# Kernel tuning notes

Hardware: AMD Instinct MI355X
Metric: run time of the kernel (lower is better)

Reference implementation:

```python
import jax, jax.numpy as jnp
import numpy as np

NSAMPLE = 64
RADIUS = 0.05
HMIN = -0.02
HMAX_LIST = (0.01, 0.02, 0.03, 0.04)
BN_EPS = 1e-5
MLP_DIMS = (3, 64, 128, 256)


def setup_inputs() -> dict:
    key = jax.random.key(0)
    ks = jax.random.split(key, 16)
    B, S, N = 2, 1024, 20000
    # points and seeds in a [0,0.5]^3 box so 0.05-radius cylinders are non-empty
    seed_xyz = jax.random.uniform(ks[0], (B, S, 3), dtype=jnp.float32) * 0.5
    pointcloud = jax.random.uniform(ks[1], (B, N, 3), dtype=jnp.float32) * 0.5
    m = jax.random.normal(ks[2], (B, S, 3, 3), dtype=jnp.float32)
    vp_rot, _ = jnp.linalg.qr(m)  # proper-ish random rotations per seed
    inp = {"seed_xyz": seed_xyz, "pointcloud": pointcloud, "vp_rot": vp_rot}
    for i in range(3):
        cin, cout = MLP_DIMS[i], MLP_DIMS[i + 1]
        inp[f"w{i+1}"] = jax.random.normal(ks[3 + i], (cout, cin), dtype=jnp.float32) * (1.0 / np.sqrt(cin))
        inp[f"gamma{i+1}"] = 1.0 + 0.1 * jax.random.normal(ks[6 + i], (cout,), dtype=jnp.float32)
        inp[f"beta{i+1}"] = 0.1 * jax.random.normal(ks[9 + i], (cout,), dtype=jnp.float32)
        inp[f"mean{i+1}"] = 0.1 * jax.random.normal(ks[12 + i], (cout,), dtype=jnp.float32)
        inp[f"var{i+1}"] = jax.random.uniform(ks[15], (cout,), minval=0.5, maxval=1.5, dtype=jnp.float32)
    return inp


def _cylinder_group(rel_rot, hmax):
    # rel_rot: (B, S, N, 3) point coords relative to each seed, in the seed (approach) frame.
    # Cylinder axis = x (approach vector): keep points with hmin < x < hmax and y^2+z^2 < r^2.
    N = rel_rot.shape[2]
    x, y, z = rel_rot[..., 0], rel_rot[..., 1], rel_rot[..., 2]
    mask = (y * y + z * z < RADIUS * RADIUS) & (x > HMIN) & (x < hmax)  # (B,S,N)
    # first NSAMPLE valid indices (ascending), padded with the first valid index (0 if none)
    score = jnp.where(mask, jnp.arange(N, dtype=jnp.int32), N)
    neg_vals, _ = jax.lax.top_k(-score, NSAMPLE)
    idx = -neg_vals  # (B,S,NSAMPLE), value N marks missing
    first = jnp.where(idx[..., :1] >= N, 0, idx[..., :1])
    idx = jnp.where(idx >= N, first, idx)
    return jnp.take_along_axis(rel_rot, idx[..., None], axis=2)  # (B,S,NSAMPLE,3)


def _bn_relu(h, gamma, beta, mean, var):
    inv = gamma / jnp.sqrt(var + BN_EPS)
    s = inv[None, :, None, None]
    b = (beta - mean * inv)[None, :, None, None]
    return jax.nn.relu(h * s + b)


def _forward(seed_xyz, pointcloud, vp_rot, layers):
    B, S, _ = seed_xyz.shape
    D = len(HMAX_LIST)
    rel = pointcloud[:, None, :, :] - seed_xyz[:, :, None, :]        # (B,S,N,3)
    rel_rot = jnp.einsum('bsnc,bscd->bsnd', rel, vp_rot)             # rotate into seed frame (rel @ rot)
    grouped = jnp.stack([_cylinder_group(rel_rot, h) for h in HMAX_LIST], axis=2)  # (B,S,D,ns,3)
    feat = jnp.transpose(grouped, (0, 4, 1, 2, 3)).reshape(B, 3, S * D, NSAMPLE)   # (B,3,S*D,ns)
    for (w, g, be, m, v) in layers:
        feat = _bn_relu(jnp.einsum('oc,bcpn->bopn', w, feat), g, be, m, v)
    vp = jnp.max(feat, axis=-1)                                       # max-pool over nsample
    return vp.reshape(B, -1, S, D)                                    # (B,256,S,D)


def reference(seed_xyz, pointcloud, vp_rot,
              w1, gamma1, beta1, mean1, var1,
              w2, gamma2, beta2, mean2, var2,
              w3, gamma3, beta3, mean3, var3):
    layers = [(w1, gamma1, beta1, mean1, var1),
              (w2, gamma2, beta2, mean2, var2),
              (w3, gamma3, beta3, mean3, var3)]
    return _forward(seed_xyz, pointcloud, vp_rot, layers)
```

## Files before the change

kernel.cpp:

```cpp
#include <hip/hip_runtime.h>

#define NPTS   20000
#define NCHUNK 313

typedef __bf16 bf16x8 __attribute__((ext_vector_type(8)));
typedef float  f32x4  __attribute__((ext_vector_type(4)));

__device__ __forceinline__ unsigned short f2b(float f) {
    __bf16 h = (__bf16)f;
    union { __bf16 h; unsigned short s; } u; u.h = h; return u.s;
}
__device__ __forceinline__ unsigned int pk2(float a, float b) {
    return (unsigned int)f2b(a) | ((unsigned int)f2b(b) << 16);
}

#define WS_BINNED    0
#define WS_PARTHIST  640000
#define WS_COUNTS    721920
#define WS_OFFSETS   726016
#define WS_FLAGS     730112
#define WS_W2P       730368
#define WS_W3P       746752
#define WS_W1E       812288
#define WS_B1E       813056
#define WS_B2E       813312
#define WS_B3E       813824


__global__ __launch_bounds__(512)
void hist_prepack_kernel(const float* __restrict__ pointcloud,
                const float* __restrict__ w1,
                const float* __restrict__ g1,  const float* __restrict__ be1,
                const float* __restrict__ mn1, const float* __restrict__ vr1,
                const float* __restrict__ w2,
                const float* __restrict__ g2,  const float* __restrict__ be2,
                const float* __restrict__ mn2, const float* __restrict__ vr2,
                const float* __restrict__ w3,
                const float* __restrict__ g3,  const float* __restrict__ be3,
                const float* __restrict__ mn3, const float* __restrict__ vr3,
                unsigned int* __restrict__ parthist,
                unsigned short* __restrict__ w2p,
                unsigned short* __restrict__ w3p,
                float* __restrict__ w1e_g, float* __restrict__ b1e_g,
                float* __restrict__ b2e_g, float* __restrict__ b3e_g)
{
    __shared__ unsigned int h[512];
    const int blk = blockIdx.x;
    const int b   = blk / 20;
    const int p   = blk % 20;
    const int tid = threadIdx.x;
    const int gid = blk * 512 + tid;

    for (int e = gid; e < 8192; e += 20480) {
        int row = e >> 6;
        float inv = g2[row] / sqrtf(vr2[row] + 1e-5f);
        w2p[e] = f2b(w2[e] * inv);
    }
    for (int e = gid; e < 32768; e += 20480) {
        int row = e >> 7;
        float inv = g3[row] / sqrtf(vr3[row] + 1e-5f);
        w3p[e] = f2b(w3[e] * inv);
    }
    if (gid < 64) {
        float inv = g1[gid] / sqrtf(vr1[gid] + 1e-5f);
        w1e_g[gid*3+0] = inv * w1[gid*3+0];
        w1e_g[gid*3+1] = inv * w1[gid*3+1];
        w1e_g[gid*3+2] = inv * w1[gid*3+2];
        b1e_g[gid]     = be1[gid] - mn1[gid] * inv;
    }
    if (gid < 128) {
        float inv = g2[gid] / sqrtf(vr2[gid] + 1e-5f);
        b2e_g[gid] = be2[gid] - mn2[gid] * inv;
    }
    if (gid < 256) {
        float inv = g3[gid] / sqrtf(vr3[gid] + 1e-5f);
        b3e_g[gid] = be3[gid] - mn3[gid] * inv;
    }

    h[tid] = 0;
    __syncthreads();

    const float* base = pointcloud + (b * NPTS + p * 1000) * 3;
    for (int i = tid; i < 1000; i += 512) {
        float x = base[i*3+0], y = base[i*3+1], z = base[i*3+2];
        int cx = min(7, (int)(x * 16.0f));
        int cy = min(7, (int)(y * 16.0f));
        int cz = min(7, (int)(z * 16.0f));
        atomicAdd(&h[(cz * 8 + cy) * 8 + cx], 1u);
    }
    __syncthreads();

    parthist[blk * 512 + tid] = h[tid];
}

__global__ __launch_bounds__(512)
void scan_kernel(const unsigned int* __restrict__ parthist,
                 unsigned int* __restrict__ counts,
                 unsigned int* __restrict__ offsets)
{
    __shared__ unsigned int scanv[512];
    const int b   = blockIdx.x;
    const int tid = threadIdx.x;

    unsigned int cnt = 0;
    #pragma unroll
    for (int pp = 0; pp < 20; ++pp)
        cnt += parthist[(b * 20 + pp) * 512 + tid];

    scanv[tid] = cnt;
    __syncthreads();
    #pragma unroll
    for (int off = 1; off < 512; off <<= 1) {
        unsigned int v = 0;
        if (tid >= off) v = scanv[tid - off];
        __syncthreads();
        scanv[tid] += v;
        __syncthreads();
    }
    unsigned int excl = scanv[tid] - cnt;
    counts [b * 512 + tid] = cnt;
    offsets[b * 512 + tid] = b * NPTS + excl;
}

__global__ __launch_bounds__(512)
void scatter_kernel(const float* __restrict__ pointcloud,
                    const unsigned int* __restrict__ parthist,
                    const unsigned int* __restrict__ offsets,
                    float4* __restrict__ binned)
{
    __shared__ unsigned int cur[512];
    const int blk = blockIdx.x;
    const int b   = blk / 20;
    const int p   = blk % 20;
    const int tid = threadIdx.x;

    unsigned int partial = 0;
    for (int pp = 0; pp < p; ++pp)
        partial += parthist[(b * 20 + pp) * 512 + tid];
    cur[tid] = offsets[b * 512 + tid] + partial;
    __syncthreads();

    const float* base = pointcloud + (b * NPTS + p * 1000) * 3;
    for (int i = tid; i < 1000; i += 512) {
        float x = base[i*3+0], y = base[i*3+1], z = base[i*3+2];
        int cx = min(7, (int)(x * 16.0f));
        int cy = min(7, (int)(y * 16.0f));
        int cz = min(7, (int)(z * 16.0f));
        int cid = (cz * 8 + cy) * 8 + cx;
        unsigned int slot = atomicAdd(&cur[cid], 1u);
        binned[slot] = make_float4(x, y, z, __int_as_float(p * 1000 + i));
    }
}

struct __align__(16) SMemF {
    union {
        struct {
            unsigned int bm[4][640];
            int cstart[64];
            int ccnt[64];
        } a;
        struct {
            unsigned short h1[64][72];
            unsigned short h2[64][136];
        } b;
    } u;
    int    idxs[4][64];
    float  w1e[64][3];
    float  b1e[64];
};

__global__ __launch_bounds__(256, 2)
void fused_kernel(const float* __restrict__ seed_xyz,
                  const float* __restrict__ pointcloud,
                  const float* __restrict__ vp_rot,
                  const unsigned int* __restrict__ counts,
                  const unsigned int* __restrict__ offsets,
                  const float4* __restrict__ binned,
                  const unsigned short* __restrict__ w2p,
                  const unsigned short* __restrict__ w3p,
                  const float* __restrict__ w1e_g, const float* __restrict__ b1e_g,
                  const float* __restrict__ b2e_g, const float* __restrict__ b3e_g,
                  float* __restrict__ out)
{
    __shared__ SMemF sm;
    const int tid = threadIdx.x;
    const int wv  = tid >> 6;
    const int ln  = tid & 63;
    const int q   = ln >> 4;
    const int l15 = ln & 15;

    const int blk = blockIdx.x;
    const int i8  = blk >> 3;
    const int s   = (blk & 7) * 128 + (i8 & 127);
    const int b   = i8 >> 7;
    const int bs  = b * 1024 + s;

    if (tid < 64) {
        sm.w1e[tid][0] = w1e_g[tid*3+0];
        sm.w1e[tid][1] = w1e_g[tid*3+1];
        sm.w1e[tid][2] = w1e_g[tid*3+2];
        sm.b1e[tid]    = b1e_g[tid];
    }

    {
        unsigned int* bmp = &sm.u.a.bm[0][0];
        #pragma unroll
        for (int i = 0; i < 10; ++i) bmp[tid + i * 256] = 0;
    }

    const float sx = seed_xyz[bs*3+0];
    const float sy = seed_xyz[bs*3+1];
    const float sz = seed_xyz[bs*3+2];
    const float R00 = vp_rot[bs*9+0], R01 = vp_rot[bs*9+1], R02 = vp_rot[bs*9+2];
    const float R10 = vp_rot[bs*9+3], R11 = vp_rot[bs*9+4], R12 = vp_rot[bs*9+5];
    const float R20 = vp_rot[bs*9+6], R21 = vp_rot[bs*9+7], R22 = vp_rot[bs*9+8];

    const int lx = max(0, (int)floorf((sx - 0.066f) * 16.f));
    const int hx = min(7, (int)floorf((sx + 0.066f) * 16.f));
    const int ly = max(0, (int)floorf((sy - 0.066f) * 16.f));
    const int hy = min(7, (int)floorf((sy + 0.066f) * 16.f));
    const int lz = max(0, (int)floorf((sz - 0.066f) * 16.f));
    const int hz = min(7, (int)floorf((sz + 0.066f) * 16.f));
    const int nx = hx - lx + 1, ny = hy - ly + 1, nz = hz - lz + 1;
    const int ncell = nx * ny * nz;

    if (tid < ncell) {
        int cz = lz + tid / (nx * ny);
        int rem = tid % (nx * ny);
        int cy = ly + rem / nx;
        int cx = lx + rem % nx;
        int cid = (cz * 8 + cy) * 8 + cx;
        sm.u.a.cstart[tid] = (int)offsets[b * 512 + cid];
        sm.u.a.ccnt[tid]   = (int)counts [b * 512 + cid];
    }
    __syncthreads();

    {
        #pragma clang fp contract(off)
        for (int k = wv; k < ncell; k += 4) {
            const int base = sm.u.a.cstart[k];
            const int cnt  = sm.u.a.ccnt[k];
            for (int i = ln; i < cnt; i += 64) {
                float4 pt = binned[base + i];
                float rx = pt.x - sx, ry = pt.y - sy, rz = pt.z - sz;
                float x = (rx*R00 + ry*R10) + rz*R20;
                float y = (rx*R01 + ry*R11) + rz*R21;
                float z = (rx*R02 + ry*R12) + rz*R22;
                if (((y*y + z*z) < 0.0025f) && (x > -0.02f) && (x < 0.04f)) {
                    int n = __float_as_int(pt.w);
                    unsigned int bit = 1u << (n & 31);
                    int wi = n >> 5;
                    if (x < 0.01f) atomicOr(&sm.u.a.bm[0][wi], bit);
                    if (x < 0.02f) atomicOr(&sm.u.a.bm[1][wi], bit);
                    if (x < 0.03f) atomicOr(&sm.u.a.bm[2][wi], bit);
                    atomicOr(&sm.u.a.bm[3][wi], bit);
                }
            }
        }
    }
    __syncthreads();

    {
        const int d = wv;
        int carry = 0;
        for (int r = 0; r < 5 && carry < 64; ++r) {
            int c = r*64 + ln;
            unsigned long long w = 0ULL;
            if (c < NCHUNK)
                w = ((unsigned long long)sm.u.a.bm[d][2*c+1] << 32)
                  |  (unsigned long long)sm.u.a.bm[d][2*c];
            int wc = __popcll(w);
            int incl = wc;
            #pragma unroll
            for (int off = 1; off < 64; off <<= 1) {
                int t = __shfl_up(incl, off);
                if (ln >= off) incl += t;
            }
            int rank  = carry + incl - wc;
            int total = __shfl(incl, 63);
            while (w && rank < 64) {
                int bp = __builtin_ctzll(w);
                w &= w - 1;
                sm.idxs[d][rank] = c*64 + bp;
                ++rank;
            }
            carry += total;
        }
        int cnt = carry < 64 ? carry : 64;
        int first = (cnt > 0) ? sm.idxs[d][0] : 0;
        if (ln >= cnt) sm.idxs[d][ln] = first;
    }

    bf16x8 aw2[2][2];
    #pragma unroll
    for (int m = 0; m < 2; ++m) {
        int row = (wv*2+m)*16 + l15;
        #pragma unroll
        for (int kk = 0; kk < 2; ++kk)
            aw2[m][kk] = *(const bf16x8*)(w2p + row*64 + kk*32 + q*8);
    }

    __syncthreads();

    auto do_l1 = [&](int d) {
        int n = sm.idxs[d][ln];
        const float* p = pointcloud + (b*NPTS + n)*3;
        float x0, x1, x2;
        {
            #pragma clang fp contract(off)
            float rx = p[0] - sx, ry = p[1] - sy, rz = p[2] - sz;
            x0 = (rx*R00 + ry*R10) + rz*R20;
            x1 = (rx*R01 + ry*R11) + rz*R21;
            x2 = (rx*R02 + ry*R12) + rz*R22;
        }
        unsigned int pk[8];
        #pragma unroll
        for (int i = 0; i < 8; ++i) {
            int ch = wv*16 + i*2;
            float ha = fmaf(x0, sm.w1e[ch][0],
                       fmaf(x1, sm.w1e[ch][1],
                       fmaf(x2, sm.w1e[ch][2], sm.b1e[ch])));
            float hb = fmaf(x0, sm.w1e[ch+1][0],
                       fmaf(x1, sm.w1e[ch+1][1],
                       fmaf(x2, sm.w1e[ch+1][2], sm.b1e[ch+1])));
            pk[i] = pk2(fmaxf(ha, 0.f), fmaxf(hb, 0.f));
        }
        *(uint4*)&sm.u.b.h1[ln][wv*16 + 0] = make_uint4(pk[0], pk[1], pk[2], pk[3]);
        *(uint4*)&sm.u.b.h1[ln][wv*16 + 8] = make_uint4(pk[4], pk[5], pk[6], pk[7]);
    };

    do_l1(0);
    __syncthreads();

    for (int d = 0; d < 4; ++d) {
        {
            f32x4 binit2[2];
            #pragma unroll
            for (int m = 0; m < 2; ++m)
                binit2[m] = *(const f32x4*)&b2e_g[(wv*2+m)*16 + q*4];
            #pragma unroll
            for (int nt = 0; nt < 4; ++nt) {
                int n = nt*16 + l15;
                bf16x8 b0 = *(const bf16x8*)&sm.u.b.h1[n][q*8];
                bf16x8 b1 = *(const bf16x8*)&sm.u.b.h1[n][32 + q*8];
                #pragma unroll
                for (int m = 0; m < 2; ++m) {
                    f32x4 acc = binit2[m];
                    acc = __builtin_amdgcn_mfma_f32_16x16x32_bf16(aw2[m][0], b0, acc, 0, 0, 0);
                    acc = __builtin_amdgcn_mfma_f32_16x16x32_bf16(aw2[m][1], b1, acc, 0, 0, 0);
                    int ch0 = (wv*2+m)*16 + q*4;
                    uint2 pkk;
                    pkk.x = pk2(fmaxf(acc[0], 0.f), fmaxf(acc[1], 0.f));
                    pkk.y = pk2(fmaxf(acc[2], 0.f), fmaxf(acc[3], 0.f));
                    *(uint2*)&sm.u.b.h2[n][ch0] = pkk;
                }
            }
        }
        __syncthreads();

        {
            float rm[4][4];
            #pragma unroll
            for (int m = 0; m < 4; ++m) {
                int row = (wv*4+m)*16 + l15;
                bf16x8 a0 = *(const bf16x8*)(w3p + row*128 +  0 + q*8);
                bf16x8 a1 = *(const bf16x8*)(w3p + row*128 + 32 + q*8);
                bf16x8 a2 = *(const bf16x8*)(w3p + row*128 + 64 + q*8);
                bf16x8 a3 = *(const bf16x8*)(w3p + row*128 + 96 + q*8);
                f32x4 binit3 = *(const f32x4*)&b3e_g[(wv*4+m)*16 + q*4];
                #pragma unroll
                for (int r = 0; r < 4; ++r) rm[m][r] = 0.f;
                #pragma unroll
                for (int nt = 0; nt < 4; ++nt) {
                    int n = nt*16 + l15;
                    bf16x8 bb0 = *(const bf16x8*)&sm.u.b.h2[n][ 0 + q*8];
                    bf16x8 bb1 = *(const bf16x8*)&sm.u.b.h2[n][32 + q*8];
                    bf16x8 bb2 = *(const bf16x8*)&sm.u.b.h2[n][64 + q*8];
                    bf16x8 bb3 = *(const bf16x8*)&sm.u.b.h2[n][96 + q*8];
                    f32x4 acc = binit3;
                    acc = __builtin_amdgcn_mfma_f32_16x16x32_bf16(a0, bb0, acc, 0, 0, 0);
                    acc = __builtin_amdgcn_mfma_f32_16x16x32_bf16(a1, bb1, acc, 0, 0, 0);
                    acc = __builtin_amdgcn_mfma_f32_16x16x32_bf16(a2, bb2, acc, 0, 0, 0);
                    acc = __builtin_amdgcn_mfma_f32_16x16x32_bf16(a3, bb3, acc, 0, 0, 0);
                    #pragma unroll
                    for (int r = 0; r < 4; ++r)
                        rm[m][r] = fmaxf(rm[m][r], acc[r]);
                }
            }

            if (d < 3) do_l1(d + 1);

            #pragma unroll
            for (int m = 0; m < 4; ++m) {
                #pragma unroll
                for (int r = 0; r < 4; ++r) {
                    float v = rm[m][r];
                    v = fmaxf(v, __shfl_xor(v, 1));
                    v = fmaxf(v, __shfl_xor(v, 2));
                    v = fmaxf(v, __shfl_xor(v, 4));
                    v = fmaxf(v, __shfl_xor(v, 8));
                    if (l15 == 0) {
                        int ch = (wv*4+m)*16 + q*4 + r;
                        out[((b*256 + ch)*1024 + s)*4 + d] = v;
                    }
                }
            }
        }
        if (d < 3) __syncthreads();
    }
}

extern "C" void kernel_launch(void* const* d_in, const int* in_sizes, int n_in,
                              void* d_out, int out_size, void* d_ws, size_t ws_size,
                              hipStream_t stream) {
    (void)in_sizes; (void)n_in; (void)out_size; (void)ws_size;
    const float* seed = (const float*)d_in[0];
    const float* pc   = (const float*)d_in[1];
    const float* rot  = (const float*)d_in[2];
    const float* w1   = (const float*)d_in[3];
    const float* g1   = (const float*)d_in[4];
    const float* be1  = (const float*)d_in[5];
    const float* mn1  = (const float*)d_in[6];
    const float* vr1  = (const float*)d_in[7];
    const float* w2   = (const float*)d_in[8];
    const float* g2   = (const float*)d_in[9];
    const float* be2  = (const float*)d_in[10];
    const float* mn2  = (const float*)d_in[11];
    const float* vr2  = (const float*)d_in[12];
    const float* w3   = (const float*)d_in[13];
    const float* g3   = (const float*)d_in[14];
    const float* be3  = (const float*)d_in[15];
    const float* mn3  = (const float*)d_in[16];
    const float* vr3  = (const float*)d_in[17];

    char* ws = (char*)d_ws;
    float4*         binned   = (float4*)(ws + WS_BINNED);
    unsigned int*   parthist = (unsigned int*)(ws + WS_PARTHIST);
    unsigned int*   counts   = (unsigned int*)(ws + WS_COUNTS);
    unsigned int*   offsets  = (unsigned int*)(ws + WS_OFFSETS);
    unsigned short* w2p      = (unsigned short*)(ws + WS_W2P);
    unsigned short* w3p      = (unsigned short*)(ws + WS_W3P);
    float*          w1e_g    = (float*)(ws + WS_W1E);
    float*          b1e_g    = (float*)(ws + WS_B1E);
    float*          b2e_g    = (float*)(ws + WS_B2E);
    float*          b3e_g    = (float*)(ws + WS_B3E);

    hist_prepack_kernel<<<dim3(40), dim3(512), 0, stream>>>(
        pc,
        w1, g1, be1, mn1, vr1,
        w2, g2, be2, mn2, vr2,
        w3, g3, be3, mn3, vr3,
        parthist,
        w2p, w3p, w1e_g, b1e_g, b2e_g, b3e_g);
    scan_kernel   <<<dim3(2),  dim3(512), 0, stream>>>(parthist, counts, offsets);
    scatter_kernel<<<dim3(40), dim3(512), 0, stream>>>(pc, parthist, offsets, binned);
    fused_kernel  <<<dim3(2048), dim3(256), 0, stream>>>(
        seed, pc, rot, counts, offsets, binned,
        w2p, w3p, w1e_g, b1e_g, b2e_g, b3e_g,
        (float*)d_out);
}
```

Before: 213.9 us.

## Merge scan into scatter kernel and cut fused-kernel register pressure for occupancy

Each of the 40 scatter blocks now recomputes the per-batch prefix scan itself, which removes the separate scan launch. Block p==0 writes counts and offsets for the fused kernel. The fused kernel's launch bounds go from 2 to 5 blocks per SIMD. To fit that budget, the layer-2 weights are reloaded per tile instead of held in registers, the layer-3 max accumulators are reduced and stored per m-tile, and the next layer-1 computation moves after the output writes. This trades redundant scan work and extra weight loads for fewer launches and higher occupancy, with a possible risk of spills.

```diff
diff --git a/kernel.cpp b/kernel.cpp
--- a/kernel.cpp
+++ b/kernel.cpp
@@ -94,19 +94,26 @@
 }
 
 __global__ __launch_bounds__(512)
-void scan_kernel(const unsigned int* __restrict__ parthist,
-                 unsigned int* __restrict__ counts,
-                 unsigned int* __restrict__ offsets)
+void scatter_kernel(const float* __restrict__ pointcloud,
+                    const unsigned int* __restrict__ parthist,
+                    unsigned int* __restrict__ counts,
+                    unsigned int* __restrict__ offsets,
+                    float4* __restrict__ binned)
 {
     __shared__ unsigned int scanv[512];
-    const int b   = blockIdx.x;
+    __shared__ unsigned int cur[512];
+    const int blk = blockIdx.x;
+    const int b   = blk / 20;
+    const int p   = blk % 20;
     const int tid = threadIdx.x;
 
-    unsigned int cnt = 0;
+    unsigned int cnt = 0, partial = 0;
     #pragma unroll
-    for (int pp = 0; pp < 20; ++pp)
-        cnt += parthist[(b * 20 + pp) * 512 + tid];
-
+    for (int pp = 0; pp < 20; ++pp) {
+        unsigned int v = parthist[(b * 20 + pp) * 512 + tid];
+        cnt += v;
+        if (pp < p) partial += v;
+    }
     scanv[tid] = cnt;
     __syncthreads();
     #pragma unroll
@@ -118,26 +125,11 @@
         __syncthreads();
     }
     unsigned int excl = scanv[tid] - cnt;
-    counts [b * 512 + tid] = cnt;
-    offsets[b * 512 + tid] = b * NPTS + excl;
-}
-
-__global__ __launch_bounds__(512)
-void scatter_kernel(const float* __restrict__ pointcloud,
-                    const unsigned int* __restrict__ parthist,
-                    const unsigned int* __restrict__ offsets,
-                    float4* __restrict__ binned)
-{
-    __shared__ unsigned int cur[512];
-    const int blk = blockIdx.x;
-    const int b   = blk / 20;
-    const int p   = blk % 20;
-    const int tid = threadIdx.x;
-
-    unsigned int partial = 0;
-    for (int pp = 0; pp < p; ++pp)
-        partial += parthist[(b * 20 + pp) * 512 + tid];
-    cur[tid] = offsets[b * 512 + tid] + partial;
+    if (p == 0) {
+        counts [b * 512 + tid] = cnt;
+        offsets[b * 512 + tid] = b * NPTS + excl;
+    }
+    cur[tid] = b * NPTS + excl + partial;
     __syncthreads();
 
     const float* base = pointcloud + (b * NPTS + p * 1000) * 3;
@@ -169,7 +161,7 @@
     float  b1e[64];
 };
 
-__global__ __launch_bounds__(256, 2)
+__global__ __launch_bounds__(256, 5)
 void fused_kernel(const float* __restrict__ seed_xyz,
                   const float* __restrict__ pointcloud,
                   const float* __restrict__ vp_rot,
@@ -291,15 +283,6 @@
         if (ln >= cnt) sm.idxs[d][ln] = first;
     }
 
-    bf16x8 aw2[2][2];
-    #pragma unroll
-    for (int m = 0; m < 2; ++m) {
-        int row = (wv*2+m)*16 + l15;
-        #pragma unroll
-        for (int kk = 0; kk < 2; ++kk)
-            aw2[m][kk] = *(const bf16x8*)(w2p + row*64 + kk*32 + q*8);
-    }
-
     __syncthreads();
 
     auto do_l1 = [&](int d) {
@@ -334,20 +317,20 @@
 
     for (int d = 0; d < 4; ++d) {
         {
-            f32x4 binit2[2];
             #pragma unroll
-            for (int m = 0; m < 2; ++m)
-                binit2[m] = *(const f32x4*)&b2e_g[(wv*2+m)*16 + q*4];
-            #pragma unroll
-            for (int nt = 0; nt < 4; ++nt) {
-                int n = nt*16 + l15;
-                bf16x8 b0 = *(const bf16x8*)&sm.u.b.h1[n][q*8];
-                bf16x8 b1 = *(const bf16x8*)&sm.u.b.h1[n][32 + q*8];
+            for (int m = 0; m < 2; ++m) {
+                int row = (wv*2+m)*16 + l15;
+                bf16x8 a0 = *(const bf16x8*)(w2p + row*64 +  0 + q*8);
+                bf16x8 a1 = *(const bf16x8*)(w2p + row*64 + 32 + q*8);
+                f32x4 binit2 = *(const f32x4*)&b2e_g[(wv*2+m)*16 + q*4];
                 #pragma unroll
-                for (int m = 0; m < 2; ++m) {
-                    f32x4 acc = binit2[m];
-                    acc = __builtin_amdgcn_mfma_f32_16x16x32_bf16(aw2[m][0], b0, acc, 0, 0, 0);
-                    acc = __builtin_amdgcn_mfma_f32_16x16x32_bf16(aw2[m][1], b1, acc, 0, 0, 0);
+                for (int nt = 0; nt < 4; ++nt) {
+                    int n = nt*16 + l15;
+                    bf16x8 b0 = *(const bf16x8*)&sm.u.b.h1[n][q*8];
+                    bf16x8 b1 = *(const bf16x8*)&sm.u.b.h1[n][32 + q*8];
+                    f32x4 acc = binit2;
+                    acc = __builtin_amdgcn_mfma_f32_16x16x32_bf16(a0, b0, acc, 0, 0, 0);
+                    acc = __builtin_amdgcn_mfma_f32_16x16x32_bf16(a1, b1, acc, 0, 0, 0);
                     int ch0 = (wv*2+m)*16 + q*4;
                     uint2 pkk;
                     pkk.x = pk2(fmaxf(acc[0], 0.f), fmaxf(acc[1], 0.f));
@@ -359,7 +342,6 @@
         __syncthreads();
 
         {
-            float rm[4][4];
             #pragma unroll
             for (int m = 0; m < 4; ++m) {
                 int row = (wv*4+m)*16 + l15;
@@ -368,8 +350,9 @@
                 bf16x8 a2 = *(const bf16x8*)(w3p + row*128 + 64 + q*8);
                 bf16x8 a3 = *(const bf16x8*)(w3p + row*128 + 96 + q*8);
                 f32x4 binit3 = *(const f32x4*)&b3e_g[(wv*4+m)*16 + q*4];
+                float rm[4];
                 #pragma unroll
-                for (int r = 0; r < 4; ++r) rm[m][r] = 0.f;
+                for (int r = 0; r < 4; ++r) rm[r] = 0.f;
                 #pragma unroll
                 for (int nt = 0; nt < 4; ++nt) {
                     int n = nt*16 + l15;
@@ -384,17 +367,11 @@
                     acc = __builtin_amdgcn_mfma_f32_16x16x32_bf16(a3, bb3, acc, 0, 0, 0);
                     #pragma unroll
                     for (int r = 0; r < 4; ++r)
-                        rm[m][r] = fmaxf(rm[m][r], acc[r]);
+                        rm[r] = fmaxf(rm[r], acc[r]);
                 }
-            }
-
-            if (d < 3) do_l1(d + 1);
-
-            #pragma unroll
-            for (int m = 0; m < 4; ++m) {
                 #pragma unroll
                 for (int r = 0; r < 4; ++r) {
-                    float v = rm[m][r];
+                    float v = rm[r];
                     v = fmaxf(v, __shfl_xor(v, 1));
                     v = fmaxf(v, __shfl_xor(v, 2));
                     v = fmaxf(v, __shfl_xor(v, 4));
@@ -405,6 +382,8 @@
                     }
                 }
             }
+
+            if (d < 3) do_l1(d + 1);
         }
         if (d < 3) __syncthreads();
     }
@@ -452,8 +431,8 @@
         w3, g3, be3, mn3, vr3,
         parthist,
         w2p, w3p, w1e_g, b1e_g, b2e_g, b3e_g);
-    scan_kernel   <<<dim3(2),  dim3(512), 0, stream>>>(parthist, counts, offsets);
-    scatter_kernel<<<dim3(40), dim3(512), 0, stream>>>(pc, parthist, offsets, binned);
+    scatter_kernel<<<dim3(40), dim3(512), 0, stream>>>(
+        pc, parthist, counts, offsets, binned);
     fused_kernel  <<<dim3(2048), dim3(256), 0, stream>>>(
         seed, pc, rot, counts, offsets, binned,
         w2p, w3p, w1e_g, b1e_g, b2e_g, b3e_g,
```

After: 448.9 us. 110% more time.
